# Kernel tuning notes

Hardware: AMD Instinct MI355X
Metric: run time of the kernel (lower is better)

The kernel has to match this reference:

```python
import jax, jax.numpy as jnp
import numpy as np

EPS = 1e-5

def bn(x, g, b):
    # training-mode BatchNorm2d: normalize over all axes except channel axis 1
    ax = (0,) + tuple(range(2, x.ndim))
    m = x.mean(ax, keepdims=True)
    v = x.var(ax, keepdims=True)
    sh = (1, -1) + (1,) * (x.ndim - 2)
    return (x - m) * jax.lax.rsqrt(v + EPS) * g.reshape(sh) + b.reshape(sh)

def setup_inputs():
    key = jax.random.key(0)
    ks = jax.random.split(key, 7)
    N, C, H, W, G = 2, 128, 128, 128, 8
    gp = C // G  # group_planes = 16
    f32 = jnp.float32
    x = jax.random.normal(ks[0], (N, C, H, W), f32)
    wq = jax.random.normal(ks[1], (C // 2, C), f32) * np.float32(np.sqrt(1.0 / (C * gp)))
    wk = jax.random.normal(ks[2], (C // 2, C), f32) * np.float32(np.sqrt(1.0 / C))
    wv = jax.random.normal(ks[3], (C, C), f32) * np.float32(np.sqrt(1.0 / C))
    q_rel = jax.random.normal(ks[4], (gp // 2, 2 * H - 1), f32) * np.float32(np.sqrt(2.0 / C))
    k_rel = jax.random.normal(ks[5], (gp // 2, 2 * H - 1), f32) * np.float32(np.sqrt(2.0 / C))
    v_rel = jax.random.normal(ks[6], (gp, 2 * H - 1), f32) * np.float32(np.sqrt(1.0 / C))
    d = dict(x=x, wq=wq, wk=wk, wv=wv, q_rel=q_rel, k_rel=k_rel, v_rel=v_rel)
    for name, ch in [("bnq", C // 2), ("bnk", C // 2), ("bnv", C), ("bnqk", G), ("bnqr", G), ("bnkr", G), ("bnsv", C), ("bnsve", C)]:
        d[name + "_g"] = jnp.ones((ch,), f32)
        d[name + "_b"] = jnp.zeros((ch,), f32)
    return d

def reference(x, wq, wk, wv, q_rel, k_rel, v_rel, bnq_g, bnq_b, bnk_g, bnk_b, bnv_g, bnv_b, bnqk_g, bnqk_b, bnqr_g, bnqr_b, bnkr_g, bnkr_b, bnsv_g, bnsv_b, bnsve_g, bnsve_b):
    N, C, H, W = x.shape
    G = 8
    gp = C // G
    # 1x1 conv == channel matmul
    q = bn(jnp.einsum('oc,bchw->bohw', wq, x), bnq_g, bnq_b)
    k = bn(jnp.einsum('oc,bchw->bohw', wk, x), bnk_g, bnk_b)
    v = bn(jnp.einsum('oc,bchw->bohw', wv, x), bnv_g, bnv_b)
    # relative embedding gather: emb[c, j, i] = rel[c, j - i + H - 1]
    idx = jnp.arange(H)[:, None] - jnp.arange(H)[None, :] + (H - 1)  # [H, H]
    q_emb = q_rel[:, idx]
    k_emb = k_rel[:, idx]
    v_emb = v_rel[:, idx]
    qg = q.reshape(N, G, gp // 2, H, W)
    kg = k.reshape(N, G, gp // 2, H, W)
    vg = v.reshape(N, G, gp, H, W)
    qr = jnp.einsum('bgciw,cij->bgijw', qg, q_emb)
    qr = bn(qr.reshape(N, G, H * H, W), bnqr_g, bnqr_b).reshape(N, G, H, H, W)
    kr = jnp.einsum('bgciw,cij->bgijw', kg, k_emb)
    kr = bn(kr.reshape(N, G, H * H, W), bnkr_g, bnkr_b).reshape(N, G, H, H, W)
    kr = kr.transpose(0, 1, 3, 2, 4)
    qk = jnp.einsum('bgciw,bgcjw->bgijw', qg, kg)
    qk = bn(qk.reshape(N, G, H * H, W), bnqk_g, bnqk_b).reshape(N, G, H, H, W)
    sim = jax.nn.softmax(qk + qr + kr, axis=3)  # [N, G, H(i), H(j), W]
    sv = jnp.einsum('bgijw,bgcjw->bgciw', sim, vg).reshape(N, C, H, W)
    sve = jnp.einsum('bgijw,cji->bgciw', sim, v_emb).reshape(N, C, H, W)
    return bn(sv, bnsv_g, bnsv_b) + bn(sve, bnsve_g, bnsve_b)
```

## Files before the change

kernel.cpp:

```cpp
#include <hip/hip_runtime.h>


#define HW 16384

__device__ __forceinline__ float warp_sum(float v) {
#pragma unroll
  for (int o = 32; o > 0; o >>= 1) v += __shfl_down(v, o);
  return v;
}

__global__ __launch_bounds__(256) void k_transpose(const float* __restrict__ in, float* __restrict__ out) {
  __shared__ float t[32][33];
  int plane = blockIdx.y;
  int th = (blockIdx.x >> 2) * 32;
  int tw = (blockIdx.x & 3) * 32;
  const float* p = in + (size_t)plane * HW;
  float* q = out + (size_t)plane * HW;
  int lx = threadIdx.x, ly = threadIdx.y;
#pragma unroll
  for (int r = ly; r < 32; r += 8) t[r][lx] = p[(th + r) * 128 + tw + lx];
  __syncthreads();
#pragma unroll
  for (int r = ly; r < 32; r += 8) q[(tw + r) * 128 + th + lx] = t[lx][r];
}

__global__ __launch_bounds__(256) void k_wT(const float* __restrict__ wq, const float* __restrict__ wk,
                                            const float* __restrict__ wv, float* __restrict__ WT) {
  int idx = blockIdx.x * 256 + threadIdx.x;
  int och = idx & 255, c = idx >> 8;
  const float* wrow = och < 64 ? wq + och * 128 : (och < 128 ? wk + (och - 64) * 128 : wv + (och - 128) * 128);
  WT[c * 256 + och] = wrow[c];
}

__global__ __launch_bounds__(256) void k_qkv(const float* __restrict__ xT, const float* __restrict__ WT,
                                             float* __restrict__ qkvT) {
  __shared__ float Xs[128][64];
  __shared__ float Ws[128][64];
  int pb = blockIdx.x * 64;
  int ob = blockIdx.y * 64;
  int b = blockIdx.z;
  const float* xb = xT + (size_t)b * (128 * HW);
  int tid = threadIdx.x;
  for (int idx = tid; idx < 8192; idx += 256) {
    int c = idx >> 6, p = idx & 63;
    Xs[c][p] = xb[c * HW + pb + p];
  }
  for (int idx = tid; idx < 8192; idx += 256) {
    int c = idx >> 6, o = idx & 63;
    Ws[c][o] = WT[c * 256 + ob + o];
  }
  __syncthreads();
  int tx = tid & 15, ty = tid >> 4;
  float acc[4][4] = {};
#pragma unroll 8
  for (int kk = 0; kk < 128; ++kk) {
    float a0 = Ws[kk][ty * 4 + 0], a1 = Ws[kk][ty * 4 + 1], a2 = Ws[kk][ty * 4 + 2], a3 = Ws[kk][ty * 4 + 3];
    float4 bv = *reinterpret_cast<const float4*>(&Xs[kk][tx * 4]);
    acc[0][0] += a0 * bv.x; acc[0][1] += a0 * bv.y; acc[0][2] += a0 * bv.z; acc[0][3] += a0 * bv.w;
    acc[1][0] += a1 * bv.x; acc[1][1] += a1 * bv.y; acc[1][2] += a1 * bv.z; acc[1][3] += a1 * bv.w;
    acc[2][0] += a2 * bv.x; acc[2][1] += a2 * bv.y; acc[2][2] += a2 * bv.z; acc[2][3] += a2 * bv.w;
    acc[3][0] += a3 * bv.x; acc[3][1] += a3 * bv.y; acc[3][2] += a3 * bv.z; acc[3][3] += a3 * bv.w;
  }
#pragma unroll
  for (int r = 0; r < 4; ++r) {
    int row = ob + ty * 4 + r;
    float4 o4 = make_float4(acc[r][0], acc[r][1], acc[r][2], acc[r][3]);
    *reinterpret_cast<float4*>(&qkvT[(size_t)(b * 256 + row) * HW + pb + tx * 4]) = o4;
  }
}

__global__ __launch_bounds__(256) void k_qkv_stats(const float* __restrict__ qkvT, double* __restrict__ statsQKV) {
  __shared__ float r1[4], r2[4];
  int ch = blockIdx.x;
  float s = 0.f, s2 = 0.f;
  for (int b = 0; b < 2; ++b) {
    const float* p = qkvT + (size_t)(b * 256 + ch) * HW;
    for (int idx = threadIdx.x; idx < HW; idx += 256) { float v = p[idx]; s += v; s2 += v * v; }
  }
  s = warp_sum(s); s2 = warp_sum(s2);
  int wid = threadIdx.x >> 6;
  if ((threadIdx.x & 63) == 0) { r1[wid] = s; r2[wid] = s2; }
  __syncthreads();
  if (threadIdx.x == 0) {
    statsQKV[2 * ch]     = (double)(r1[0] + r1[1] + r1[2] + r1[3]);
    statsQKV[2 * ch + 1] = (double)(r2[0] + r2[1] + r2[2] + r2[3]);
  }
}

__global__ __launch_bounds__(128) void k_rel_tables(const float* __restrict__ q_rel, const float* __restrict__ k_rel,
                                                    float* __restrict__ tabs) {
  int tbl = blockIdx.x / 44, item = blockIdx.x % 44;
  const float* rel = tbl ? k_rel : q_rel;
  float* out = tabs + tbl * 5632;
  int i = threadIdx.x;
  float s = 0.f;
  if (item < 8) {
    const float* r = rel + item * 255 + i;
    for (int d = 0; d < 128; ++d) s += r[d];
  } else {
    int p = item - 8;
    int pp = p, c = 0;
    while (pp >= 8 - c) { pp -= 8 - c; ++c; }
    int c2 = c + pp;
    const float* ra = rel + c * 255 + i;
    const float* rb = rel + c2 * 255 + i;
    for (int d = 0; d < 128; ++d) s += ra[d] * rb[d];
  }
  out[item * 128 + i] = s;
}

__global__ __launch_bounds__(128) void k_qkr_stats(
    const float* __restrict__ qkvT, const double* __restrict__ statsQKV,
    const float* __restrict__ bnq_g, const float* __restrict__ bnq_b,
    const float* __restrict__ bnk_g, const float* __restrict__ bnk_b,
    const float* __restrict__ tabs, double* __restrict__ statsA) {
  __shared__ float red[92][2];
  int slice = blockIdx.x;
  int w = slice & 127, g = (slice >> 7) & 7, b = slice >> 10;
  int i = threadIdx.x;
  float qn[8], kn[8];
  const float* qbase = qkvT + (size_t)(b * 256 + g * 8) * HW + w * 128 + i;
  const float* kbase = qkvT + (size_t)(b * 256 + 64 + g * 8) * HW + w * 128 + i;
#pragma unroll
  for (int c = 0; c < 8; ++c) {
    {
      int och = g * 8 + c;
      double su = statsQKV[2 * och], sq = statsQKV[2 * och + 1];
      double mu = su * (1.0 / 32768.0);
      float var = (float)(sq * (1.0 / 32768.0) - mu * mu);
      float sc = bnq_g[och] * rsqrtf(var + 1e-5f);
      qn[c] = qbase[c * HW] * sc + (bnq_b[och] - (float)mu * sc);
    }
    {
      int gi = g * 8 + c, och = 64 + gi;
      double su = statsQKV[2 * och], sq = statsQKV[2 * och + 1];
      double mu = su * (1.0 / 32768.0);
      float var = (float)(sq * (1.0 / 32768.0) - mu * mu);
      float sc = bnk_g[gi] * rsqrtf(var + 1e-5f);
      kn[c] = kbase[c * HW] * sc + (bnk_b[gi] - (float)mu * sc);
    }
  }
  float vals[92];
  int n = 0;
#pragma unroll
  for (int c = 0; c < 8; ++c) vals[n++] = qn[c];
#pragma unroll
  for (int c = 0; c < 8; ++c) vals[n++] = kn[c];
#pragma unroll
  for (int c = 0; c < 8; ++c)
#pragma unroll
    for (int c2 = c; c2 < 8; ++c2) vals[n++] = qn[c] * qn[c2];
#pragma unroll
  for (int c = 0; c < 8; ++c)
#pragma unroll
    for (int c2 = c; c2 < 8; ++c2) vals[n++] = kn[c] * kn[c2];
  float sqr = 0.f, s2qr = 0.f, skr = 0.f, s2kr = 0.f;
#pragma unroll
  for (int c = 0; c < 8; ++c) {
    sqr += qn[c] * tabs[c * 128 + i];
    skr += kn[c] * tabs[5632 + c * 128 + i];
  }
  {
    int p = 0;
#pragma unroll
    for (int c = 0; c < 8; ++c)
#pragma unroll
      for (int c2 = c; c2 < 8; ++c2) {
        float f = (c == c2) ? 1.f : 2.f;
        s2qr += f * qn[c] * qn[c2] * tabs[1024 + p * 128 + i];
        s2kr += f * kn[c] * kn[c2] * tabs[5632 + 1024 + p * 128 + i];
        ++p;
      }
  }
  vals[88] = sqr; vals[89] = s2qr; vals[90] = skr; vals[91] = s2kr;
  int lane = i & 63, wid = i >> 6;
#pragma unroll
  for (int vv = 0; vv < 92; ++vv) {
    float r = warp_sum(vals[vv]);
    if (lane == 0) red[vv][wid] = r;
  }
  __syncthreads();
  if (i == 0) {
    float f[92];
#pragma unroll
    for (int vv = 0; vv < 92; ++vv) f[vv] = red[vv][0] + red[vv][1];
    float sS = 0.f, s2S = 0.f;
#pragma unroll
    for (int c = 0; c < 8; ++c) sS += f[c] * f[8 + c];
    {
      int p = 0;
#pragma unroll
      for (int c = 0; c < 8; ++c)
#pragma unroll
        for (int c2 = c; c2 < 8; ++c2) { float fm = (c == c2) ? 1.f : 2.f; s2S += fm * f[16 + p] * f[52 + p]; ++p; }
    }
    atomicAdd(&statsA[(0 * 8 + g) * 2 + 0], (double)sS);
    atomicAdd(&statsA[(0 * 8 + g) * 2 + 1], (double)s2S);
    atomicAdd(&statsA[(1 * 8 + g) * 2 + 0], (double)f[88]);
    atomicAdd(&statsA[(1 * 8 + g) * 2 + 1], (double)f[89]);
    atomicAdd(&statsA[(2 * 8 + g) * 2 + 0], (double)f[90]);
    atomicAdd(&statsA[(2 * 8 + g) * 2 + 1], (double)f[91]);
  }
}

__global__ __launch_bounds__(256) void k_relT(const float* __restrict__ q_rel, const float* __restrict__ k_rel,
                                              float* __restrict__ relT) {
  int idx = blockIdx.x * 256 + threadIdx.x;
  if (idx < 2040) {
    int d = idx >> 3, c = idx & 7;
    relT[idx] = q_rel[c * 255 + d];
  } else if (idx < 4080) {
    int j = idx - 2040;
    int d = j >> 3, c = j & 7;
    relT[2040 + j] = k_rel[c * 255 + d];
  }
}

__global__ __launch_bounds__(256, 4) void k_attn(
    const float* __restrict__ qkvT,
    const double* __restrict__ statsQKV, const double* __restrict__ statsA,
    const float* __restrict__ relTq, const float* __restrict__ relTk, const float* __restrict__ v_rel,
    const float* __restrict__ bnq_g, const float* __restrict__ bnq_b,
    const float* __restrict__ bnk_g, const float* __restrict__ bnk_b,
    const float* __restrict__ bnv_g, const float* __restrict__ bnv_b,
    const float* __restrict__ bnqk_g, const float* __restrict__ bnqk_b,
    const float* __restrict__ bnqr_g, const float* __restrict__ bnqr_b,
    const float* __restrict__ bnkr_g, const float* __restrict__ bnkr_b,
    float* __restrict__ svT, float* __restrict__ sveT) {
  __shared__ float Ks[128][8];
  __shared__ float Vs[128][16];
  __shared__ float Wr[255][20];
  __shared__ float nsc[32], nsh[32];
  int slice = blockIdx.x;
  int w = slice & 127, g = (slice >> 7) & 7, b = slice >> 10;
  int tid = threadIdx.x;
  if (tid < 32) {
    int och, gi; const float* gm; const float* bt;
    if (tid < 8)       { gi = g * 8 + tid;        och = gi;       gm = bnq_g; bt = bnq_b; }
    else if (tid < 16) { gi = g * 8 + (tid - 8);  och = 64 + gi;  gm = bnk_g; bt = bnk_b; }
    else               { gi = g * 16 + (tid - 16); och = 128 + gi; gm = bnv_g; bt = bnv_b; }
    double su = statsQKV[2 * och], sq = statsQKV[2 * och + 1];
    double mu = su * (1.0 / 32768.0);
    float var = (float)(sq * (1.0 / 32768.0) - mu * mu);
    float sc = gm[gi] * rsqrtf(var + 1e-5f);
    nsc[tid] = sc;
    nsh[tid] = bt[gi] - (float)mu * sc;
  }
  __syncthreads();
  {
    const float* kbase = qkvT + (size_t)(b * 256 + 64 + g * 8) * HW + w * 128;
    for (int idx = tid; idx < 1024; idx += 256) {
      int c = idx >> 7, jj = idx & 127;
      Ks[jj][c] = kbase[c * HW + jj] * nsc[8 + c] + nsh[8 + c];
    }
    const float* vbase = qkvT + (size_t)(b * 256 + 128 + g * 16) * HW + w * 128;
    for (int idx = tid; idx < 2048; idx += 256) {
      int c = idx >> 7, jj = idx & 127;
      Vs[jj][c] = vbase[c * HW + jj] * nsc[16 + c] + nsh[16 + c];
    }
    for (int idx = tid; idx < 4096; idx += 256) {
      int c = idx >> 8, t = idx & 255;
      if (t < 255) Wr[t][c] = v_rel[c * 255 + t];
    }
  }
  int i = tid >> 1, h = tid & 1;
  float qreg[8];
  {
    const float* qbase = qkvT + (size_t)(b * 256 + g * 8) * HW + w * 128;
#pragma unroll
    for (int c = 0; c < 8; ++c) qreg[c] = qbase[c * HW + i] * nsc[c] + nsh[c];
  }
  float aS, aQR, aKR, offs;
  {
    const double inv = 1.0 / 4194304.0;
    double s0 = statsA[(0 * 8 + g) * 2], q0 = statsA[(0 * 8 + g) * 2 + 1];
    double s1 = statsA[(1 * 8 + g) * 2], q1 = statsA[(1 * 8 + g) * 2 + 1];
    double s2 = statsA[(2 * 8 + g) * 2], q2 = statsA[(2 * 8 + g) * 2 + 1];
    double m0 = s0 * inv, m1 = s1 * inv, m2 = s2 * inv;
    float v0 = (float)(q0 * inv - m0 * m0);
    float v1 = (float)(q1 * inv - m1 * m1);
    float v2 = (float)(q2 * inv - m2 * m2);
    aS  = bnqk_g[g] * rsqrtf(v0 + 1e-5f);
    aQR = bnqr_g[g] * rsqrtf(v1 + 1e-5f);
    aKR = bnkr_g[g] * rsqrtf(v2 + 1e-5f);
    offs = (bnqk_b[g] - (float)m0 * aS) + (bnqr_b[g] - (float)m1 * aQR) + (bnkr_b[g] - (float)m2 * aKR);
  }
  __syncthreads();

  const int jbase = h << 6;
  float l = 0.f;
  float asv[16] = {}, asve[16] = {};
  const float* qrp = relTq + (size_t)(127 + i - jbase) * 8;
  const float* krp = relTk + (size_t)(127 - i + jbase) * 8;
  const float* wp  = &Wr[127 - i + jbase][0];
  const float* kp  = &Ks[jbase][0];
  const float* vp  = &Vs[jbase][0];

  for (int jj = 0; jj < 64; ++jj) {
    float4 ka = *reinterpret_cast<const float4*>(kp);
    float4 kb = *reinterpret_cast<const float4*>(kp + 4);
    float4 qa = *reinterpret_cast<const float4*>(qrp);
    float4 qb = *reinterpret_cast<const float4*>(qrp + 4);
    float4 ra = *reinterpret_cast<const float4*>(krp);
    float4 rb = *reinterpret_cast<const float4*>(krp + 4);
    float S  = qreg[0] * ka.x + qreg[1] * ka.y + qreg[2] * ka.z + qreg[3] * ka.w
             + qreg[4] * kb.x + qreg[5] * kb.y + qreg[6] * kb.z + qreg[7] * kb.w;
    float QR = qreg[0] * qa.x + qreg[1] * qa.y + qreg[2] * qa.z + qreg[3] * qa.w
             + qreg[4] * qb.x + qreg[5] * qb.y + qreg[6] * qb.z + qreg[7] * qb.w;
    float KR = ka.x * ra.x + ka.y * ra.y + ka.z * ra.z + ka.w * ra.w
             + kb.x * rb.x + kb.y * rb.y + kb.z * rb.z + kb.w * rb.w;
    float a = fmaf(S, aS, fmaf(QR, aQR, fmaf(KR, aKR, offs)));
    float e = __expf(a);
    l += e;
    float4 v0 = *reinterpret_cast<const float4*>(vp);
    float4 v1 = *reinterpret_cast<const float4*>(vp + 4);
    float4 v2 = *reinterpret_cast<const float4*>(vp + 8);
    float4 v3 = *reinterpret_cast<const float4*>(vp + 12);
    float4 w0 = *reinterpret_cast<const float4*>(wp);
    float4 w1 = *reinterpret_cast<const float4*>(wp + 4);
    float4 w2 = *reinterpret_cast<const float4*>(wp + 8);
    float4 w3 = *reinterpret_cast<const float4*>(wp + 12);
    asv[0]  += e * v0.x; asv[1]  += e * v0.y; asv[2]  += e * v0.z; asv[3]  += e * v0.w;
    asv[4]  += e * v1.x; asv[5]  += e * v1.y; asv[6]  += e * v1.z; asv[7]  += e * v1.w;
    asv[8]  += e * v2.x; asv[9]  += e * v2.y; asv[10] += e * v2.z; asv[11] += e * v2.w;
    asv[12] += e * v3.x; asv[13] += e * v3.y; asv[14] += e * v3.z; asv[15] += e * v3.w;
    asve[0]  += e * w0.x; asve[1]  += e * w0.y; asve[2]  += e * w0.z; asve[3]  += e * w0.w;
    asve[4]  += e * w1.x; asve[5]  += e * w1.y; asve[6]  += e * w1.z; asve[7]  += e * w1.w;
    asve[8]  += e * w2.x; asve[9]  += e * w2.y; asve[10] += e * w2.z; asve[11] += e * w2.w;
    asve[12] += e * w3.x; asve[13] += e * w3.y; asve[14] += e * w3.z; asve[15] += e * w3.w;
    qrp -= 8; krp += 8; wp += 20; kp += 8; vp += 16;
  }
  float L = l + __shfl_xor(l, 1);
  float linv = 1.f / L;
  float* outp = (h ? sveT : svT) + (size_t)slice * 2048 + i;
#pragma unroll
  for (int c = 0; c < 16; ++c) {
    float vsv = asv[c] + __shfl_xor(asv[c], 1);
    float vse = asve[c] + __shfl_xor(asve[c], 1);
    outp[c * 128] = (h ? vse : vsv) * linv;
  }
}

__global__ __launch_bounds__(256) void k_sv_stats(const float* __restrict__ svT, const float* __restrict__ sveT,
                                                  double* __restrict__ statsSV) {
  __shared__ float r1[4], r2[4];
  int ch = blockIdx.x;
  const float* base = (ch < 128) ? svT : sveT;
  int c = ch & 127, g = c >> 4, cc = c & 15;
  float s = 0.f, s2 = 0.f;
  for (int idx = threadIdx.x; idx < 32768; idx += 256) {
    int bw = idx >> 7, ii = idx & 127;
    int bb = bw >> 7, wwi = bw & 127;
    float v = base[(size_t)(((bb * 8 + g) * 128) + wwi) * 2048 + cc * 128 + ii];
    s += v; s2 += v * v;
  }
  s = warp_sum(s); s2 = warp_sum(s2);
  int wid = threadIdx.x >> 6;
  if ((threadIdx.x & 63) == 0) { r1[wid] = s; r2[wid] = s2; }
  __syncthreads();
  if (threadIdx.x == 0) {
    statsSV[2 * ch]     = (double)(r1[0] + r1[1] + r1[2] + r1[3]);
    statsSV[2 * ch + 1] = (double)(r2[0] + r2[1] + r2[2] + r2[3]);
  }
}

__global__ __launch_bounds__(256) void k_final(const float* __restrict__ svT, const float* __restrict__ sveT,
                                               const double* __restrict__ statsSV,
                                               const float* __restrict__ bnsv_g, const float* __restrict__ bnsv_b,
                                               const float* __restrict__ bnsve_g, const float* __restrict__ bnsve_b,
                                               float* __restrict__ out) {
  __shared__ float t[32][33];
  int plane = blockIdx.y;
  int b = plane >> 7, c = plane & 127;
  int g = c >> 4, cc = c & 15;
  double s = statsSV[2 * c], s2 = statsSV[2 * c + 1];
  double mu1 = s * (1.0 / 32768.0);
  float var1 = (float)(s2 * (1.0 / 32768.0) - mu1 * mu1);
  float sc1 = bnsv_g[c] * rsqrtf(var1 + 1e-5f);
  float sh1 = bnsv_b[c] - (float)mu1 * sc1;
  double se = statsSV[2 * (128 + c)], se2 = statsSV[2 * (128 + c) + 1];
  double mu2 = se * (1.0 / 32768.0);
  float var2 = (float)(se2 * (1.0 / 32768.0) - mu2 * mu2);
  float sc2 = bnsve_g[c] * rsqrtf(var2 + 1e-5f);
  float sh2 = bnsve_b[c] - (float)mu2 * sc2;
  int tw = (blockIdx.x & 3) * 32, ti = (blockIdx.x >> 2) * 32;
  int lx = threadIdx.x, ly = threadIdx.y;
#pragma unroll
  for (int r = ly; r < 32; r += 8) {
    int wr = tw + r, ii = ti + lx;
    size_t off = (size_t)((b * 8 + g) * 128 + wr) * 2048 + cc * 128 + ii;
    t[r][lx] = svT[off] * sc1 + sh1 + sveT[off] * sc2 + sh2;
  }
  __syncthreads();
#pragma unroll
  for (int r = ly; r < 32; r += 8)
    out[(size_t)plane * HW + (ti + r) * 128 + tw + lx] = t[lx][r];
}

extern "C" void kernel_launch(void* const* d_in, const int* in_sizes, int n_in,
                              void* d_out, int out_size, void* d_ws, size_t ws_size,
                              hipStream_t stream) {
  const float* x      = (const float*)d_in[0];
  const float* wq     = (const float*)d_in[1];
  const float* wk     = (const float*)d_in[2];
  const float* wv     = (const float*)d_in[3];
  const float* q_rel  = (const float*)d_in[4];
  const float* k_rel  = (const float*)d_in[5];
  const float* v_rel  = (const float*)d_in[6];
  const float* bnq_g  = (const float*)d_in[7];
  const float* bnq_b  = (const float*)d_in[8];
  const float* bnk_g  = (const float*)d_in[9];
  const float* bnk_b  = (const float*)d_in[10];
  const float* bnv_g  = (const float*)d_in[11];
  const float* bnv_b  = (const float*)d_in[12];
  const float* bnqk_g = (const float*)d_in[13];
  const float* bnqk_b = (const float*)d_in[14];
  const float* bnqr_g = (const float*)d_in[15];
  const float* bnqr_b = (const float*)d_in[16];
  const float* bnkr_g = (const float*)d_in[17];
  const float* bnkr_b = (const float*)d_in[18];
  const float* bnsv_g = (const float*)d_in[19];
  const float* bnsv_b = (const float*)d_in[20];
  const float* bnsve_g = (const float*)d_in[21];
  const float* bnsve_b = (const float*)d_in[22];
  float* out = (float*)d_out;

  float* wsf  = (float*)d_ws;
  float* xT   = wsf;
  float* svT  = wsf;
  float* qkvT = wsf + 4194304;
  float* sveT = wsf + 12582912;
  float* tabs = wsf + 16777216;
  float* relTq = tabs;
  float* relTk = tabs + 2040;
  float* WT   = wsf + 16788480;
  double* statsQKV = (double*)(wsf + 16821248);
  double* statsA   = statsQKV + 512;
  double* statsSV  = statsA + 48;

  hipMemsetAsync(statsA, 0, 48 * sizeof(double), stream);
  k_transpose<<<dim3(16, 256), dim3(32, 8), 0, stream>>>(x, xT);
  k_wT<<<128, 256, 0, stream>>>(wq, wk, wv, WT);
  k_qkv<<<dim3(256, 4, 2), 256, 0, stream>>>(xT, WT, qkvT);
  k_qkv_stats<<<256, 256, 0, stream>>>(qkvT, statsQKV);
  k_rel_tables<<<88, 128, 0, stream>>>(q_rel, k_rel, tabs);
  k_qkr_stats<<<2048, 128, 0, stream>>>(qkvT, statsQKV, bnq_g, bnq_b, bnk_g, bnk_b, tabs, statsA);
  k_relT<<<16, 256, 0, stream>>>(q_rel, k_rel, relTq);
  k_attn<<<2048, 256, 0, stream>>>(qkvT, statsQKV, statsA, relTq, relTk, v_rel,
                                   bnq_g, bnq_b, bnk_g, bnk_b, bnv_g, bnv_b,
                                   bnqk_g, bnqk_b, bnqr_g, bnqr_b, bnkr_g, bnkr_b,
                                   svT, sveT);
  k_sv_stats<<<256, 256, 0, stream>>>(svT, sveT, statsSV);
  k_final<<<dim3(16, 256), dim3(32, 8), 0, stream>>>(svT, sveT, statsSV,
                                                     bnsv_g, bnsv_b, bnsve_g, bnsve_b, out);
  (void)in_sizes; (void)n_in; (void)out_size; (void)ws_size;
}
```

Baseline: 448.9 us.

## Use packed fp16 for the positional-value accumulation and split the QKV K-loop

In the attention kernel, the v_rel table in shared memory is stored as half. The sve accumulation now uses packed half2 FMAs, which halves the FMA count and the LDS traffic for that half of the work. The exponent argument is shifted down by ln(256) so the fp16 accumulators are less likely to overflow; the shift cancels in the softmax normalisation. The min-blocks launch bound is dropped and the inner loop is unrolled by 2. The QKV GEMM now stages K in two 64-wide chunks to halve shared memory and raise occupancy. Accumulating in fp16 risks a loss of accuracy on the sve output.

```diff
diff --git a/kernel.cpp b/kernel.cpp
--- a/kernel.cpp
+++ b/kernel.cpp
@@ -1,4 +1,5 @@
 #include <hip/hip_runtime.h>
+#include <hip/hip_fp16.h>
 
 
 #define HW 16384
@@ -34,32 +35,35 @@
 
 __global__ __launch_bounds__(256) void k_qkv(const float* __restrict__ xT, const float* __restrict__ WT,
                                              float* __restrict__ qkvT) {
-  __shared__ float Xs[128][64];
-  __shared__ float Ws[128][64];
+  __shared__ float Xs[64][64];
+  __shared__ float Ws[64][64];
   int pb = blockIdx.x * 64;
   int ob = blockIdx.y * 64;
   int b = blockIdx.z;
   const float* xb = xT + (size_t)b * (128 * HW);
   int tid = threadIdx.x;
-  for (int idx = tid; idx < 8192; idx += 256) {
-    int c = idx >> 6, p = idx & 63;
-    Xs[c][p] = xb[c * HW + pb + p];
-  }
-  for (int idx = tid; idx < 8192; idx += 256) {
-    int c = idx >> 6, o = idx & 63;
-    Ws[c][o] = WT[c * 256 + ob + o];
-  }
-  __syncthreads();
   int tx = tid & 15, ty = tid >> 4;
   float acc[4][4] = {};
+  for (int ks = 0; ks < 2; ++ks) {
+    for (int idx = tid; idx < 4096; idx += 256) {
+      int c = idx >> 6, p = idx & 63;
+      Xs[c][p] = xb[(ks * 64 + c) * HW + pb + p];
+    }
+    for (int idx = tid; idx < 4096; idx += 256) {
+      int c = idx >> 6, o = idx & 63;
+      Ws[c][o] = WT[(ks * 64 + c) * 256 + ob + o];
+    }
+    __syncthreads();
 #pragma unroll 8
-  for (int kk = 0; kk < 128; ++kk) {
-    float a0 = Ws[kk][ty * 4 + 0], a1 = Ws[kk][ty * 4 + 1], a2 = Ws[kk][ty * 4 + 2], a3 = Ws[kk][ty * 4 + 3];
-    float4 bv = *reinterpret_cast<const float4*>(&Xs[kk][tx * 4]);
-    acc[0][0] += a0 * bv.x; acc[0][1] += a0 * bv.y; acc[0][2] += a0 * bv.z; acc[0][3] += a0 * bv.w;
-    acc[1][0] += a1 * bv.x; acc[1][1] += a1 * bv.y; acc[1][2] += a1 * bv.z; acc[1][3] += a1 * bv.w;
-    acc[2][0] += a2 * bv.x; acc[2][1] += a2 * bv.y; acc[2][2] += a2 * bv.z; acc[2][3] += a2 * bv.w;
-    acc[3][0] += a3 * bv.x; acc[3][1] += a3 * bv.y; acc[3][2] += a3 * bv.z; acc[3][3] += a3 * bv.w;
+    for (int kk = 0; kk < 64; ++kk) {
+      float a0 = Ws[kk][ty * 4 + 0], a1 = Ws[kk][ty * 4 + 1], a2 = Ws[kk][ty * 4 + 2], a3 = Ws[kk][ty * 4 + 3];
+      float4 bv = *reinterpret_cast<const float4*>(&Xs[kk][tx * 4]);
+      acc[0][0] += a0 * bv.x; acc[0][1] += a0 * bv.y; acc[0][2] += a0 * bv.z; acc[0][3] += a0 * bv.w;
+      acc[1][0] += a1 * bv.x; acc[1][1] += a1 * bv.y; acc[1][2] += a1 * bv.z; acc[1][3] += a1 * bv.w;
+      acc[2][0] += a2 * bv.x; acc[2][1] += a2 * bv.y; acc[2][2] += a2 * bv.z; acc[2][3] += a2 * bv.w;
+      acc[3][0] += a3 * bv.x; acc[3][1] += a3 * bv.y; acc[3][2] += a3 * bv.z; acc[3][3] += a3 * bv.w;
+    }
+    __syncthreads();
   }
 #pragma unroll
   for (int r = 0; r < 4; ++r) {
@@ -216,7 +220,7 @@
   }
 }
 
-__global__ __launch_bounds__(256, 4) void k_attn(
+__global__ __launch_bounds__(256) void k_attn(
     const float* __restrict__ qkvT,
     const double* __restrict__ statsQKV, const double* __restrict__ statsA,
     const float* __restrict__ relTq, const float* __restrict__ relTk, const float* __restrict__ v_rel,
@@ -229,7 +233,7 @@
     float* __restrict__ svT, float* __restrict__ sveT) {
   __shared__ float Ks[128][8];
   __shared__ float Vs[128][16];
-  __shared__ float Wr[255][20];
+  __shared__ __half Wr[255 * 20];
   __shared__ float nsc[32], nsh[32];
   int slice = blockIdx.x;
   int w = slice & 127, g = (slice >> 7) & 7, b = slice >> 10;
@@ -259,8 +263,8 @@
       Vs[jj][c] = vbase[c * HW + jj] * nsc[16 + c] + nsh[16 + c];
     }
     for (int idx = tid; idx < 4096; idx += 256) {
-      int c = idx >> 8, t = idx & 255;
-      if (t < 255) Wr[t][c] = v_rel[c * 255 + t];
+      int c = idx >> 8, d = idx & 255;
+      if (d < 255) Wr[d * 20 + c] = __float2half(v_rel[c * 255 + d]);
     }
   }
   int i = tid >> 1, h = tid & 1;
@@ -284,18 +288,23 @@
     aQR = bnqr_g[g] * rsqrtf(v1 + 1e-5f);
     aKR = bnkr_g[g] * rsqrtf(v2 + 1e-5f);
     offs = (bnqk_b[g] - (float)m0 * aS) + (bnqr_b[g] - (float)m1 * aQR) + (bnkr_b[g] - (float)m2 * aKR);
+    offs -= 5.545177444479562f;
   }
   __syncthreads();
 
   const int jbase = h << 6;
   float l = 0.f;
-  float asv[16] = {}, asve[16] = {};
+  float asv[16] = {};
+  __half2 hacc[8];
+#pragma unroll
+  for (int u = 0; u < 8; ++u) hacc[u] = __float2half2_rn(0.f);
   const float* qrp = relTq + (size_t)(127 + i - jbase) * 8;
   const float* krp = relTk + (size_t)(127 - i + jbase) * 8;
-  const float* wp  = &Wr[127 - i + jbase][0];
+  const __half* wp = Wr + (127 - i + jbase) * 20;
   const float* kp  = &Ks[jbase][0];
   const float* vp  = &Vs[jbase][0];
 
+#pragma unroll 2
   for (int jj = 0; jj < 64; ++jj) {
     float4 ka = *reinterpret_cast<const float4*>(kp);
     float4 kb = *reinterpret_cast<const float4*>(kp + 4);
@@ -316,18 +325,23 @@
     float4 v1 = *reinterpret_cast<const float4*>(vp + 4);
     float4 v2 = *reinterpret_cast<const float4*>(vp + 8);
     float4 v3 = *reinterpret_cast<const float4*>(vp + 12);
-    float4 w0 = *reinterpret_cast<const float4*>(wp);
-    float4 w1 = *reinterpret_cast<const float4*>(wp + 4);
-    float4 w2 = *reinterpret_cast<const float4*>(wp + 8);
-    float4 w3 = *reinterpret_cast<const float4*>(wp + 12);
     asv[0]  += e * v0.x; asv[1]  += e * v0.y; asv[2]  += e * v0.z; asv[3]  += e * v0.w;
     asv[4]  += e * v1.x; asv[5]  += e * v1.y; asv[6]  += e * v1.z; asv[7]  += e * v1.w;
     asv[8]  += e * v2.x; asv[9]  += e * v2.y; asv[10] += e * v2.z; asv[11] += e * v2.w;
     asv[12] += e * v3.x; asv[13] += e * v3.y; asv[14] += e * v3.z; asv[15] += e * v3.w;
-    asve[0]  += e * w0.x; asve[1]  += e * w0.y; asve[2]  += e * w0.z; asve[3]  += e * w0.w;
-    asve[4]  += e * w1.x; asve[5]  += e * w1.y; asve[6]  += e * w1.z; asve[7]  += e * w1.w;
-    asve[8]  += e * w2.x; asve[9]  += e * w2.y; asve[10] += e * w2.z; asve[11] += e * w2.w;
-    asve[12] += e * w3.x; asve[13] += e * w3.y; asve[14] += e * w3.z; asve[15] += e * w3.w;
+    __half2 eh2 = __float2half2_rn(e);
+    float2 w0 = *reinterpret_cast<const float2*>(wp);
+    float2 w1 = *reinterpret_cast<const float2*>(wp + 4);
+    float2 w2 = *reinterpret_cast<const float2*>(wp + 8);
+    float2 w3 = *reinterpret_cast<const float2*>(wp + 12);
+    const __half2* h0 = reinterpret_cast<const __half2*>(&w0);
+    const __half2* h1 = reinterpret_cast<const __half2*>(&w1);
+    const __half2* h2 = reinterpret_cast<const __half2*>(&w2);
+    const __half2* h3 = reinterpret_cast<const __half2*>(&w3);
+    hacc[0] = __hfma2(eh2, h0[0], hacc[0]); hacc[1] = __hfma2(eh2, h0[1], hacc[1]);
+    hacc[2] = __hfma2(eh2, h1[0], hacc[2]); hacc[3] = __hfma2(eh2, h1[1], hacc[3]);
+    hacc[4] = __hfma2(eh2, h2[0], hacc[4]); hacc[5] = __hfma2(eh2, h2[1], hacc[5]);
+    hacc[6] = __hfma2(eh2, h3[0], hacc[6]); hacc[7] = __hfma2(eh2, h3[1], hacc[7]);
     qrp -= 8; krp += 8; wp += 20; kp += 8; vp += 16;
   }
   float L = l + __shfl_xor(l, 1);
@@ -336,7 +350,8 @@
 #pragma unroll
   for (int c = 0; c < 16; ++c) {
     float vsv = asv[c] + __shfl_xor(asv[c], 1);
-    float vse = asve[c] + __shfl_xor(asve[c], 1);
+    float hv = (c & 1) ? __high2float(hacc[c >> 1]) : __low2float(hacc[c >> 1]);
+    float vse = hv + __shfl_xor(hv, 1);
     outp[c * 128] = (h ? vse : vsv) * linv;
   }
 }
```

New measurement: 455.3 us. Within noise of the previous version (+1.4%).
